# Performance work log

Hardware: AMD Instinct MI355X
Metric: run time of the kernel (lower is better)

The kernel has to match this reference:

```python
import jax, jax.numpy as jnp
import numpy as np

N_NODES = 50000
N_EDGES = 800000
IN_CH = 128
HID = 128
OUT_CH = 12
NUM_GRAPHS = 512


def _gcn_layer(x, src, dst, W, b, n):
    # GCNConv: out = D^{-1/2} (A + I) D^{-1/2} (x W) + b, messages flow src -> dst
    h = x @ W
    loops = jnp.arange(n)
    s = jnp.concatenate([src, loops])
    d = jnp.concatenate([dst, loops])
    deg = jax.ops.segment_sum(jnp.ones(s.shape[0], dtype=h.dtype), d, num_segments=n)
    dinv = jnp.where(deg > 0, jax.lax.rsqrt(deg), 0.0)
    norm = dinv[s] * dinv[d]                      # [E+N]
    msg = h[s] * norm[:, None]                    # gather + scale
    out = jax.ops.segment_sum(msg, d, num_segments=n)  # scatter-add to targets
    return out + b


def setup_inputs() -> dict:
    key = jax.random.key(0)
    ks = jax.random.split(key, 12)
    x = jax.random.normal(ks[0], (N_NODES, IN_CH), dtype=jnp.float32)
    edge_index = jax.random.randint(ks[1], (2, N_EDGES), 0, N_NODES, dtype=jnp.int64)
    batch = jnp.sort(jax.random.randint(ks[2], (N_NODES,), 0, NUM_GRAPHS, dtype=jnp.int64))
    sc = 0.05
    W0 = jax.random.normal(ks[3], (IN_CH, HID), dtype=jnp.float32) * sc
    b0 = jnp.zeros((HID,), dtype=jnp.float32)
    W1 = jax.random.normal(ks[4], (HID, HID), dtype=jnp.float32) * sc
    b1 = jnp.zeros((HID,), dtype=jnp.float32)
    W2 = jax.random.normal(ks[5], (HID, HID), dtype=jnp.float32) * sc
    b2 = jnp.zeros((HID,), dtype=jnp.float32)
    Wc = jax.random.normal(ks[6], (HID, OUT_CH), dtype=jnp.float32) * sc
    bc = jnp.zeros((OUT_CH,), dtype=jnp.float32)
    return {"x": x, "edge_index": edge_index, "batch": batch,
            "W0": W0, "b0": b0, "W1": W1, "b1": b1, "W2": W2, "b2": b2,
            "Wc": Wc, "bc": bc}


def reference(x, edge_index, batch, W0, b0, W1, b1, W2, b2, Wc, bc):
    src, dst = edge_index[0], edge_index[1]
    n = x.shape[0]
    h = _gcn_layer(x, src, dst, W0, b0, n)
    h = jax.nn.relu(h)  # dropout is identity in eval mode
    h = _gcn_layer(h, src, dst, W1, b1, n)
    h = jax.nn.relu(h)
    h = _gcn_layer(h, src, dst, W2, b2, n)
    # global_mean_pool by graph id
    sums = jax.ops.segment_sum(h, batch, num_segments=NUM_GRAPHS)
    cnt = jax.ops.segment_sum(jnp.ones((n,), dtype=h.dtype), batch, num_segments=NUM_GRAPHS)
    pooled = sums / jnp.maximum(cnt, 1.0)[:, None]
    return pooled @ Wc + bc
```

## Files before the change

### kernel.cpp

```cpp
#include <hip/hip_runtime.h>
#include <hip/hip_bf16.h>


#define CH  128
#define CAP 64
#define NW  8

typedef unsigned int  uint;
typedef unsigned short ushort;

__device__ inline float bflo(uint u) { return __uint_as_float(u << 16); }
__device__ inline float bfhi(uint u) { return __uint_as_float(u & 0xffff0000u); }
__device__ inline ushort f2bf(float f) {
    uint u = __float_as_uint(f);
    return (ushort)((u + 0x7fffu + ((u >> 16) & 1u)) >> 16);
}

__global__ __launch_bounds__(256) void k_scatter(const int* __restrict__ src,
                                                 const int* __restrict__ dstv,
                                                 int* __restrict__ len,
                                                 int* __restrict__ csr_src,
                                                 int E, int nper) {
    int p = blockIdx.x & (NW - 1);
    int chunk = blockIdx.x >> 3;
    int lo = p * nper, hi = lo + nper;
    int e0 = (chunk * 256 + threadIdx.x) * 4;
    if (e0 + 3 < E) {
        int4 s4 = *(const int4*)&src[e0];
        int4 d4 = *(const int4*)&dstv[e0];
        if (d4.x >= lo && d4.x < hi) {
            int pos = atomicAdd(&len[d4.x], 1);
            if (pos < CAP) csr_src[d4.x * CAP + pos] = s4.x;
        }
        if (d4.y >= lo && d4.y < hi) {
            int pos = atomicAdd(&len[d4.y], 1);
            if (pos < CAP) csr_src[d4.y * CAP + pos] = s4.y;
        }
        if (d4.z >= lo && d4.z < hi) {
            int pos = atomicAdd(&len[d4.z], 1);
            if (pos < CAP) csr_src[d4.z * CAP + pos] = s4.z;
        }
        if (d4.w >= lo && d4.w < hi) {
            int pos = atomicAdd(&len[d4.w], 1);
            if (pos < CAP) csr_src[d4.w * CAP + pos] = s4.w;
        }
    } else {
        for (int e = e0; e < E; ++e) {
            int d = dstv[e];
            if (d >= lo && d < hi) {
                int pos = atomicAdd(&len[d], 1);
                if (pos < CAP) csr_src[d * CAP + pos] = src[e];
            }
        }
    }
}

__global__ void k_prep(const int* __restrict__ len, float* __restrict__ dinv,
                       const int* __restrict__ batch, int* __restrict__ gstart,
                       int n, int G) {
    int v = blockIdx.x * blockDim.x + threadIdx.x;
    if (v > n) return;
    if (v < n) dinv[v] = 1.0f / sqrtf((float)(len[v] + 1));
    int prev = (v == 0) ? -1 : batch[v - 1];
    int cur  = (v == n) ? G  : batch[v];
    for (int g = prev + 1; g <= cur; ++g) gstart[g] = v;
}

__global__ __launch_bounds__(256) void k_gemm(const float* __restrict__ A,
                                              const float* __restrict__ W,
                                              ushort* __restrict__ C, int M) {
    __shared__ float As[64][36];
    __shared__ float Bs[32][132];
    int tid = threadIdx.x;
    int tcol = tid & 31;
    int trow = tid >> 5;
    int row0 = blockIdx.x * 64;
    float acc[8][4] = {};
    for (int kk = 0; kk < CH; kk += 32) {
        #pragma unroll
        for (int l = 0; l < 2; ++l) {
            int idx = tid * 2 + l;
            int r = idx >> 3;
            int kp = (idx & 7) * 4;
            int grow = row0 + r;
            float4 val = (grow < M) ? *(const float4*)&A[(size_t)grow * CH + kk + kp]
                                    : make_float4(0.f, 0.f, 0.f, 0.f);
            *(float4*)&As[r][kp] = val;
        }
        #pragma unroll
        for (int l = 0; l < 4; ++l) {
            int idx = tid * 4 + l;
            int r = idx >> 5;
            int cp = (idx & 31) * 4;
            *(float4*)&Bs[r][cp] = *(const float4*)&W[(size_t)(kk + r) * CH + cp];
        }
        __syncthreads();
        #pragma unroll
        for (int k = 0; k < 32; ++k) {
            float4 b = *(const float4*)&Bs[k][tcol * 4];
            #pragma unroll
            for (int i = 0; i < 8; ++i) {
                float a = As[trow + i * 8][k];
                acc[i][0] += a * b.x; acc[i][1] += a * b.y;
                acc[i][2] += a * b.z; acc[i][3] += a * b.w;
            }
        }
        __syncthreads();
    }
    #pragma unroll
    for (int i = 0; i < 8; ++i) {
        int grow = row0 + trow + i * 8;
        if (grow < M) {
            ushort4 o;
            o.x = f2bf(acc[i][0]); o.y = f2bf(acc[i][1]);
            o.z = f2bf(acc[i][2]); o.w = f2bf(acc[i][3]);
            *(ushort4*)&C[(size_t)grow * CH + tcol * 4] = o;
        }
    }
}

__global__ __launch_bounds__(256) void k_agg(const ushort* __restrict__ T,
                                             const int* __restrict__ len,
                                             const int* __restrict__ csr_src,
                                             const float* __restrict__ dinv,
                                             const float* __restrict__ bias,
                                             float* __restrict__ out,
                                             int n, int do_relu) {
    int wid = threadIdx.x >> 6;
    int lane = threadIdx.x & 63;
    int v = blockIdx.x * 4 + wid;
    if (v >= n) return;
    int q = lane >> 4;
    int l16 = lane & 15;
    int c = l16 * 8;
    float acc[8] = {};
    int beg = v * CAP;
    int end = beg + min(len[v], CAP);
    #pragma unroll 2
    for (int p = beg + q; p < end; p += 4) {
        int s = csr_src[p];
        float w = dinv[s];
        uint4 row = *(const uint4*)&T[(size_t)s * CH + c];
        acc[0] += w * bflo(row.x); acc[1] += w * bfhi(row.x);
        acc[2] += w * bflo(row.y); acc[3] += w * bfhi(row.y);
        acc[4] += w * bflo(row.z); acc[5] += w * bfhi(row.z);
        acc[6] += w * bflo(row.w); acc[7] += w * bfhi(row.w);
    }
    #pragma unroll
    for (int j = 0; j < 8; ++j) {
        acc[j] += __shfl_xor(acc[j], 16, 64);
        acc[j] += __shfl_xor(acc[j], 32, 64);
    }
    if (q == 0) {
        float di = dinv[v];
        uint4 sv = *(const uint4*)&T[(size_t)v * CH + c];
        float s0 = bflo(sv.x), s1 = bfhi(sv.x), s2 = bflo(sv.y), s3 = bfhi(sv.y);
        float s4 = bflo(sv.z), s5 = bfhi(sv.z), s6 = bflo(sv.w), s7 = bfhi(sv.w);
        float4 ba = *(const float4*)&bias[c];
        float4 bb = *(const float4*)&bias[c + 4];
        float o0 = (acc[0] + di * s0) * di + ba.x;
        float o1 = (acc[1] + di * s1) * di + ba.y;
        float o2 = (acc[2] + di * s2) * di + ba.z;
        float o3 = (acc[3] + di * s3) * di + ba.w;
        float o4 = (acc[4] + di * s4) * di + bb.x;
        float o5 = (acc[5] + di * s5) * di + bb.y;
        float o6 = (acc[6] + di * s6) * di + bb.z;
        float o7 = (acc[7] + di * s7) * di + bb.w;
        if (do_relu) {
            o0 = fmaxf(o0, 0.f); o1 = fmaxf(o1, 0.f);
            o2 = fmaxf(o2, 0.f); o3 = fmaxf(o3, 0.f);
            o4 = fmaxf(o4, 0.f); o5 = fmaxf(o5, 0.f);
            o6 = fmaxf(o6, 0.f); o7 = fmaxf(o7, 0.f);
        }
        *(float4*)&out[(size_t)v * CH + c]     = make_float4(o0, o1, o2, o3);
        *(float4*)&out[(size_t)v * CH + c + 4] = make_float4(o4, o5, o6, o7);
    }
}

__global__ __launch_bounds__(128) void k_poolcls(const float* __restrict__ h,
                                                 const int* __restrict__ gstart,
                                                 const float* __restrict__ Wc,
                                                 const float* __restrict__ bc,
                                                 float* __restrict__ out, int OUT) {
    __shared__ float p[CH];
    int g = blockIdx.x;
    int t = threadIdx.x;
    int beg = gstart[g], end = gstart[g + 1];
    float acc = 0.f;
    for (int v = beg; v < end; ++v) acc += h[(size_t)v * CH + t];
    float cnt = fmaxf((float)(end - beg), 1.0f);
    p[t] = acc / cnt;
    __syncthreads();
    if (t < OUT) {
        float s = bc[t];
        for (int k = 0; k < CH; ++k) s += p[k] * Wc[k * OUT + t];
        out[g * OUT + t] = s;
    }
}

extern "C" void kernel_launch(void* const* d_in, const int* in_sizes, int n_in,
                              void* d_out, int out_size, void* d_ws, size_t ws_size,
                              hipStream_t stream) {
    const float* x     = (const float*)d_in[0];
    const int*   eidx  = (const int*)d_in[1];
    const int*   batch = (const int*)d_in[2];
    const float* W0 = (const float*)d_in[3];
    const float* b0 = (const float*)d_in[4];
    const float* W1 = (const float*)d_in[5];
    const float* b1 = (const float*)d_in[6];
    const float* W2 = (const float*)d_in[7];
    const float* b2 = (const float*)d_in[8];
    const float* Wc = (const float*)d_in[9];
    const float* bc = (const float*)d_in[10];
    float* out = (float*)d_out;

    const int n = in_sizes[0] / CH;
    const int E = in_sizes[1] / 2;
    const int OUT = 12;
    const int G = out_size / OUT;
    const int* src = eidx;
    const int* dst = eidx + E;

    char* ws = (char*)d_ws;
    size_t off = 0;
    auto carve = [&](size_t bytes) -> char* {
        off = (off + 255) & ~(size_t)255;
        char* p = ws + off;
        off += bytes;
        return p;
    };
    int*    len     = (int*)carve((size_t)n * 4);
    float*  dinv    = (float*)carve((size_t)n * 4);
    int*    gstart  = (int*)carve((size_t)(G + 1) * 4);
    int*    csr_src = (int*)carve((size_t)n * CAP * 4);
    ushort* T       = (ushort*)carve((size_t)n * CH * 2);
    float*  bufA    = (float*)carve((size_t)n * CH * 4);
    float*  bufB    = (float*)carve((size_t)n * CH * 4);
    (void)ws_size;

    hipMemsetAsync(len, 0, (size_t)n * 4, stream);

    const int GB = (n + 63) / 64;
    const int agg_grid = (n + 3) / 4;
    const int nper = (n + NW - 1) / NW;
    const int chunks = (E + 1023) / 1024;

    k_scatter<<<chunks * NW, 256, 0, stream>>>(src, dst, len, csr_src, E, nper);
    k_prep<<<(n + 256) / 256, 256, 0, stream>>>(len, dinv, batch, gstart, n, G);

    k_gemm<<<GB, 256, 0, stream>>>(x, W0, T, n);
    k_agg<<<agg_grid, 256, 0, stream>>>(T, len, csr_src, dinv, b0, bufB, n, 1);
    k_gemm<<<GB, 256, 0, stream>>>(bufB, W1, T, n);
    k_agg<<<agg_grid, 256, 0, stream>>>(T, len, csr_src, dinv, b1, bufA, n, 1);
    k_gemm<<<GB, 256, 0, stream>>>(bufA, W2, T, n);
    k_agg<<<agg_grid, 256, 0, stream>>>(T, len, csr_src, dinv, b2, bufB, n, 0);

    k_poolcls<<<G, CH, 0, stream>>>(bufB, gstart, Wc, bc, out, OUT);
}
```

Measured before the change: 285.6 us.

## Use bf16 MFMA GEMMs, bf16 intermediates, fused prep kernel, inline degree norm

Replaces the fp32 LDS-tiled GEMM with a bf16 MFMA 16x16x32 kernel that reads pre-transposed bf16 weights. A new prep kernel does the len zeroing, weight conversion and graph-start computation, replacing the memset and the dinv prep kernel. The dinv array is removed and degree normalization is recomputed in aggregation from len. Hidden activations between layers are stored as bf16 to halve their traffic. Scatter loads now use nontemporal hints. The cost is lower precision on inputs and intermediates, plus extra rsqrt work and scattered len reads per edge.

```diff
diff --git a/kernel.cpp b/kernel.cpp
--- a/kernel.cpp
+++ b/kernel.cpp
@@ -8,12 +8,56 @@
 
 typedef unsigned int  uint;
 typedef unsigned short ushort;
+typedef __attribute__((ext_vector_type(8))) short  short8;
+typedef __attribute__((ext_vector_type(4))) float  f32x4;
+typedef __attribute__((ext_vector_type(4))) int    i32x4;
 
 __device__ inline float bflo(uint u) { return __uint_as_float(u << 16); }
 __device__ inline float bfhi(uint u) { return __uint_as_float(u & 0xffff0000u); }
 __device__ inline ushort f2bf(float f) {
     uint u = __float_as_uint(f);
     return (ushort)((u + 0x7fffu + ((u >> 16) & 1u)) >> 16);
+}
+
+__global__ __launch_bounds__(256) void k_prep0(int4* __restrict__ len4, int nz,
+                                               const int* __restrict__ batch,
+                                               int* __restrict__ gstart, int n, int G,
+                                               const float* __restrict__ W0,
+                                               const float* __restrict__ W1,
+                                               const float* __restrict__ W2,
+                                               ushort* __restrict__ Wt0,
+                                               ushort* __restrict__ Wt1,
+                                               ushort* __restrict__ Wt2,
+                                               int ZB, int BB) {
+    int b = blockIdx.x;
+    int t = threadIdx.x;
+    if (b < ZB) {
+        int i = b * 256 + t;
+        if (i < nz) len4[i] = make_int4(0, 0, 0, 0);
+    } else if (b < ZB + BB) {
+        int v = (b - ZB) * 256 + t;
+        if (v <= n) {
+            int prev = (v == 0) ? -1 : batch[v - 1];
+            int cur  = (v == n) ? G  : batch[v];
+            for (int g = prev + 1; g <= cur; ++g) gstart[g] = v;
+        }
+    } else {
+        int m = b - ZB - BB;
+        const float* W = (m == 0) ? W0 : (m == 1) ? W1 : W2;
+        ushort* Wt = (m == 0) ? Wt0 : (m == 1) ? Wt1 : Wt2;
+        const float4* wsrc = (const float4*)W;
+        #pragma unroll
+        for (int i = 0; i < 16; ++i) {
+            int c4 = t + i * 256;
+            int k  = c4 >> 5;
+            int n0 = (c4 & 31) * 4;
+            float4 v = wsrc[c4];
+            Wt[(n0 + 0) * CH + k] = f2bf(v.x);
+            Wt[(n0 + 1) * CH + k] = f2bf(v.y);
+            Wt[(n0 + 2) * CH + k] = f2bf(v.z);
+            Wt[(n0 + 3) * CH + k] = f2bf(v.w);
+        }
+    }
 }
 
 __global__ __launch_bounds__(256) void k_scatter(const int* __restrict__ src,
@@ -26,23 +70,15 @@
     int lo = p * nper, hi = lo + nper;
     int e0 = (chunk * 256 + threadIdx.x) * 4;
     if (e0 + 3 < E) {
-        int4 s4 = *(const int4*)&src[e0];
-        int4 d4 = *(const int4*)&dstv[e0];
-        if (d4.x >= lo && d4.x < hi) {
-            int pos = atomicAdd(&len[d4.x], 1);
-            if (pos < CAP) csr_src[d4.x * CAP + pos] = s4.x;
-        }
-        if (d4.y >= lo && d4.y < hi) {
-            int pos = atomicAdd(&len[d4.y], 1);
-            if (pos < CAP) csr_src[d4.y * CAP + pos] = s4.y;
-        }
-        if (d4.z >= lo && d4.z < hi) {
-            int pos = atomicAdd(&len[d4.z], 1);
-            if (pos < CAP) csr_src[d4.z * CAP + pos] = s4.z;
-        }
-        if (d4.w >= lo && d4.w < hi) {
-            int pos = atomicAdd(&len[d4.w], 1);
-            if (pos < CAP) csr_src[d4.w * CAP + pos] = s4.w;
+        i32x4 s4 = __builtin_nontemporal_load((const i32x4*)&src[e0]);
+        i32x4 d4 = __builtin_nontemporal_load((const i32x4*)&dstv[e0]);
+        #pragma unroll
+        for (int j = 0; j < 4; ++j) {
+            int d = d4[j];
+            if (d >= lo && d < hi) {
+                int pos = atomicAdd(&len[d], 1);
+                if (pos < CAP) csr_src[d * CAP + pos] = s4[j];
+            }
         }
     } else {
         for (int e = e0; e < E; ++e) {
@@ -55,76 +91,57 @@
     }
 }
 
-__global__ void k_prep(const int* __restrict__ len, float* __restrict__ dinv,
-                       const int* __restrict__ batch, int* __restrict__ gstart,
-                       int n, int G) {
-    int v = blockIdx.x * blockDim.x + threadIdx.x;
-    if (v > n) return;
-    if (v < n) dinv[v] = 1.0f / sqrtf((float)(len[v] + 1));
-    int prev = (v == 0) ? -1 : batch[v - 1];
-    int cur  = (v == n) ? G  : batch[v];
-    for (int g = prev + 1; g <= cur; ++g) gstart[g] = v;
-}
-
-__global__ __launch_bounds__(256) void k_gemm(const float* __restrict__ A,
-                                              const float* __restrict__ W,
-                                              ushort* __restrict__ C, int M) {
-    __shared__ float As[64][36];
-    __shared__ float Bs[32][132];
+template<int IN_BF16>
+__global__ __launch_bounds__(256) void k_gemm_mfma(const void* __restrict__ Ain,
+                                                   const ushort* __restrict__ Wt,
+                                                   ushort* __restrict__ C, int M) {
     int tid = threadIdx.x;
-    int tcol = tid & 31;
-    int trow = tid >> 5;
-    int row0 = blockIdx.x * 64;
-    float acc[8][4] = {};
-    for (int kk = 0; kk < CH; kk += 32) {
-        #pragma unroll
-        for (int l = 0; l < 2; ++l) {
-            int idx = tid * 2 + l;
-            int r = idx >> 3;
-            int kp = (idx & 7) * 4;
-            int grow = row0 + r;
-            float4 val = (grow < M) ? *(const float4*)&A[(size_t)grow * CH + kk + kp]
-                                    : make_float4(0.f, 0.f, 0.f, 0.f);
-            *(float4*)&As[r][kp] = val;
-        }
-        #pragma unroll
-        for (int l = 0; l < 4; ++l) {
-            int idx = tid * 4 + l;
-            int r = idx >> 5;
-            int cp = (idx & 31) * 4;
-            *(float4*)&Bs[r][cp] = *(const float4*)&W[(size_t)(kk + r) * CH + cp];
-        }
-        __syncthreads();
-        #pragma unroll
-        for (int k = 0; k < 32; ++k) {
-            float4 b = *(const float4*)&Bs[k][tcol * 4];
-            #pragma unroll
-            for (int i = 0; i < 8; ++i) {
-                float a = As[trow + i * 8][k];
-                acc[i][0] += a * b.x; acc[i][1] += a * b.y;
-                acc[i][2] += a * b.z; acc[i][3] += a * b.w;
+    int wid = tid >> 6, lane = tid & 63;
+    int row = blockIdx.x * 64 + wid * 16 + (lane & 15);
+    int lk  = (lane >> 4) * 8;
+    bool rok = row < M;
+    f32x4 acc[8] = {};
+    #pragma unroll
+    for (int ks = 0; ks < 4; ++ks) {
+        short8 af = {};
+        if (rok) {
+            if (IN_BF16) {
+                af = *(const short8*)&((const ushort*)Ain)[(size_t)row * CH + ks * 32 + lk];
+            } else {
+                const float* Af = (const float*)Ain;
+                float4 a0 = *(const float4*)&Af[(size_t)row * CH + ks * 32 + lk];
+                float4 a1 = *(const float4*)&Af[(size_t)row * CH + ks * 32 + lk + 4];
+                af[0] = (short)f2bf(a0.x); af[1] = (short)f2bf(a0.y);
+                af[2] = (short)f2bf(a0.z); af[3] = (short)f2bf(a0.w);
+                af[4] = (short)f2bf(a1.x); af[5] = (short)f2bf(a1.y);
+                af[6] = (short)f2bf(a1.z); af[7] = (short)f2bf(a1.w);
             }
         }
-        __syncthreads();
-    }
+        #pragma unroll
+        for (int nt = 0; nt < 8; ++nt) {
+            short8 bf = *(const short8*)&Wt[(size_t)(nt * 16 + (lane & 15)) * CH + ks * 32 + lk];
+            acc[nt] = __builtin_amdgcn_mfma_f32_16x16x32_bf16(af, bf, acc[nt], 0, 0, 0);
+        }
+    }
+    int ci = (lane >> 4) * 4;
+    int cj = lane & 15;
+    int rb = blockIdx.x * 64 + wid * 16 + ci;
     #pragma unroll
-    for (int i = 0; i < 8; ++i) {
-        int grow = row0 + trow + i * 8;
-        if (grow < M) {
-            ushort4 o;
-            o.x = f2bf(acc[i][0]); o.y = f2bf(acc[i][1]);
-            o.z = f2bf(acc[i][2]); o.w = f2bf(acc[i][3]);
-            *(ushort4*)&C[(size_t)grow * CH + tcol * 4] = o;
-        }
-    }
-}
-
+    for (int nt = 0; nt < 8; ++nt) {
+        #pragma unroll
+        for (int r = 0; r < 4; ++r) {
+            int grow = rb + r;
+            if (grow < M) C[(size_t)grow * CH + nt * 16 + cj] = f2bf(acc[nt][r]);
+        }
+    }
+}
+
+template<int OB>
 __global__ __launch_bounds__(256) void k_agg(const ushort* __restrict__ T,
                                              const int* __restrict__ len,
                                              const int* __restrict__ csr_src,
-                                             const float* __restrict__ dinv,
                                              const float* __restrict__ bias,
-                                             float* __restrict__ out,
+                                             void* __restrict__ outv,
                                              int n, int do_relu) {
     int wid = threadIdx.x >> 6;
     int lane = threadIdx.x & 63;
@@ -134,12 +151,13 @@
     int l16 = lane & 15;
     int c = l16 * 8;
     float acc[8] = {};
+    int lv = len[v];
     int beg = v * CAP;
-    int end = beg + min(len[v], CAP);
+    int end = beg + min(lv, CAP);
     #pragma unroll 2
     for (int p = beg + q; p < end; p += 4) {
         int s = csr_src[p];
-        float w = dinv[s];
+        float w = 1.0f / sqrtf((float)(len[s] + 1));
         uint4 row = *(const uint4*)&T[(size_t)s * CH + c];
         acc[0] += w * bflo(row.x); acc[1] += w * bfhi(row.x);
         acc[2] += w * bflo(row.y); acc[3] += w * bfhi(row.y);
@@ -152,28 +170,35 @@
         acc[j] += __shfl_xor(acc[j], 32, 64);
     }
     if (q == 0) {
-        float di = dinv[v];
+        float di = 1.0f / sqrtf((float)(lv + 1));
         uint4 sv = *(const uint4*)&T[(size_t)v * CH + c];
         float s0 = bflo(sv.x), s1 = bfhi(sv.x), s2 = bflo(sv.y), s3 = bfhi(sv.y);
         float s4 = bflo(sv.z), s5 = bfhi(sv.z), s6 = bflo(sv.w), s7 = bfhi(sv.w);
         float4 ba = *(const float4*)&bias[c];
         float4 bb = *(const float4*)&bias[c + 4];
-        float o0 = (acc[0] + di * s0) * di + ba.x;
-        float o1 = (acc[1] + di * s1) * di + ba.y;
-        float o2 = (acc[2] + di * s2) * di + ba.z;
-        float o3 = (acc[3] + di * s3) * di + ba.w;
-        float o4 = (acc[4] + di * s4) * di + bb.x;
-        float o5 = (acc[5] + di * s5) * di + bb.y;
-        float o6 = (acc[6] + di * s6) * di + bb.z;
-        float o7 = (acc[7] + di * s7) * di + bb.w;
+        float o[8];
+        o[0] = (acc[0] + di * s0) * di + ba.x;
+        o[1] = (acc[1] + di * s1) * di + ba.y;
+        o[2] = (acc[2] + di * s2) * di + ba.z;
+        o[3] = (acc[3] + di * s3) * di + ba.w;
+        o[4] = (acc[4] + di * s4) * di + bb.x;
+        o[5] = (acc[5] + di * s5) * di + bb.y;
+        o[6] = (acc[6] + di * s6) * di + bb.z;
+        o[7] = (acc[7] + di * s7) * di + bb.w;
         if (do_relu) {
-            o0 = fmaxf(o0, 0.f); o1 = fmaxf(o1, 0.f);
-            o2 = fmaxf(o2, 0.f); o3 = fmaxf(o3, 0.f);
-            o4 = fmaxf(o4, 0.f); o5 = fmaxf(o5, 0.f);
-            o6 = fmaxf(o6, 0.f); o7 = fmaxf(o7, 0.f);
-        }
-        *(float4*)&out[(size_t)v * CH + c]     = make_float4(o0, o1, o2, o3);
-        *(float4*)&out[(size_t)v * CH + c + 4] = make_float4(o4, o5, o6, o7);
+            #pragma unroll
+            for (int j = 0; j < 8; ++j) o[j] = fmaxf(o[j], 0.f);
+        }
+        if (OB) {
+            ushort u[8];
+            #pragma unroll
+            for (int j = 0; j < 8; ++j) u[j] = f2bf(o[j]);
+            *(short8*)&((ushort*)outv)[(size_t)v * CH + c] = *(short8*)u;
+        } else {
+            float* out = (float*)outv;
+            *(float4*)&out[(size_t)v * CH + c]     = make_float4(o[0], o[1], o[2], o[3]);
+            *(float4*)&out[(size_t)v * CH + c + 4] = make_float4(o[4], o[5], o[6], o[7]);
+        }
     }
 }
 
@@ -230,30 +255,35 @@
         return p;
     };
     int*    len     = (int*)carve((size_t)n * 4);
-    float*  dinv    = (float*)carve((size_t)n * 4);
     int*    gstart  = (int*)carve((size_t)(G + 1) * 4);
+    ushort* Wt0     = (ushort*)carve((size_t)CH * CH * 2);
+    ushort* Wt1     = (ushort*)carve((size_t)CH * CH * 2);
+    ushort* Wt2     = (ushort*)carve((size_t)CH * CH * 2);
     int*    csr_src = (int*)carve((size_t)n * CAP * 4);
     ushort* T       = (ushort*)carve((size_t)n * CH * 2);
-    float*  bufA    = (float*)carve((size_t)n * CH * 4);
-    float*  bufB    = (float*)carve((size_t)n * CH * 4);
+    ushort* bufA    = (ushort*)carve((size_t)n * CH * 2);
+    ushort* bufB    = (ushort*)carve((size_t)n * CH * 2);
+    float*  bufF    = (float*)carve((size_t)n * CH * 4);
     (void)ws_size;
-
-    hipMemsetAsync(len, 0, (size_t)n * 4, stream);
 
     const int GB = (n + 63) / 64;
     const int agg_grid = (n + 3) / 4;
     const int nper = (n + NW - 1) / NW;
     const int chunks = (E + 1023) / 1024;
-
+    const int ZB = (n / 4 + 255) / 256;
+    const int BB = (n + 1 + 255) / 256;
+
+    k_prep0<<<ZB + BB + 3, 256, 0, stream>>>((int4*)len, n / 4, batch, gstart,
+                                             n, G, W0, W1, W2, Wt0, Wt1, Wt2,
+                                             ZB, BB);
     k_scatter<<<chunks * NW, 256, 0, stream>>>(src, dst, len, csr_src, E, nper);
-    k_prep<<<(n + 256) / 256, 256, 0, stream>>>(len, dinv, batch, gstart, n, G);
-
-    k_gemm<<<GB, 256, 0, stream>>>(x, W0, T, n);
-    k_agg<<<agg_grid, 256, 0, stream>>>(T, len, csr_src, dinv, b0, bufB, n, 1);
-    k_gemm<<<GB, 256, 0, stream>>>(bufB, W1, T, n);
-    k_agg<<<agg_grid, 256, 0, stream>>>(T, len, csr_src, dinv, b1, bufA, n, 1);
-    k_gemm<<<GB, 256, 0, stream>>>(bufA, W2, T, n);
-    k_agg<<<agg_grid, 256, 0, stream>>>(T, len, csr_src, dinv, b2, bufB, n, 0);
-
-    k_poolcls<<<G, CH, 0, stream>>>(bufB, gstart, Wc, bc, out, OUT);
-}
+
+    k_gemm_mfma<0><<<GB, 256, 0, stream>>>(x, Wt0, T, n);
+    k_agg<1><<<agg_grid, 256, 0, stream>>>(T, len, csr_src, b0, bufA, n, 1);
+    k_gemm_mfma<1><<<GB, 256, 0, stream>>>(bufA, Wt1, T, n);
+    k_agg<1><<<agg_grid, 256, 0, stream>>>(T, len, csr_src, b1, bufB, n, 1);
+    k_gemm_mfma<1><<<GB, 256, 0, stream>>>(bufB, Wt2, T, n);
+    k_agg<0><<<agg_grid, 256, 0, stream>>>(T, len, csr_src, b2, bufF, n, 0);
+
+    k_poolcls<<<G, CH, 0, stream>>>(bufF, gstart, Wc, bc, out, OUT);
+}
```

Result: faster. 272.0 us (-4.7%).
